# Performance work log

Measured on AMD Instinct MI355X. Metric: run time of the kernel, lower is better.

Reference implementation:

```python
import jax, jax.numpy as jnp
import numpy as np
import math

H_HEADS = 4
SQRT_2_PI = math.sqrt(2.0 / math.pi)


def _gelu_tanh(x):
    return 0.5 * x * (1.0 + jnp.tanh(SQRT_2_PI * (x + 0.044715 * x ** 3)))


def _ln(x, g, b, eps=1e-5):
    mu = jnp.mean(x, axis=-1, keepdims=True)
    var = jnp.var(x, axis=-1, keepdims=True)
    return g * (x - mu) * jax.lax.rsqrt(var + eps) + b


def _forward(support_emb_mat, query_t, support_t, cls_embed, t_freq, t_phase,
             Wq, bq, Wk, bk, Wv, bv, Wo, bo, ln1_g, ln1_b, time_w,
             W1, b1, W2, b2, ln2_g, ln2_b, Wc, bc, bn_g, bn_b):
    B, F, MD = support_emb_mat.shape
    Q = query_t.shape[1]
    S = F + 1
    H = H_HEADS
    D = MD * H
    dph = D // H
    L = Wq.shape[0]
    BQ = B * Q

    # [CLS] + support sequence, feature-tiled to model_dim*num_heads
    cls = jnp.broadcast_to(cls_embed, (B, 1, MD))
    seq = jnp.concatenate([cls, support_emb_mat], axis=1)          # [B,S,MD]
    x = jnp.tile(seq, (1, 1, H))                                    # [B,S,D]
    x = jnp.broadcast_to(x[:, None], (B, Q, S, D)).reshape(BQ, S, D)

    # time sequence: [query_t_q, support_t...] per (b,q)
    sup = jnp.broadcast_to(support_t[:, None, :], (B, Q, F))
    t_seq = jnp.concatenate([query_t[..., None], sup], axis=-1).reshape(BQ, S)
    t_diff = t_seq[:, :, None] - t_seq[:, None, :]                  # [BQ,S,S]
    # time encoder: cos(t*freq + phase) -> [BQ,S,S,TD]
    t_emb = jnp.cos(t_diff[..., None] * t_freq + t_phase)

    # scale as in source: (dim_per_head // num_heads) ** -0.5
    scale = (dph // H) ** (-0.5)

    for l in range(L):
        bias = t_emb @ time_w[l]                                    # [BQ,S,S]
        add = jnp.tile(bias, (H, 1, 1))                             # [BQ*H,S,S]
        res = x
        # raw row-major reshape to (BQ*H, S, dph) exactly as torch .view
        q = (x @ Wq[l] + bq[l]).reshape(BQ * H, S, dph)
        k = (x @ Wk[l] + bk[l]).reshape(BQ * H, S, dph)
        v = (x @ Wv[l] + bv[l]).reshape(BQ * H, S, dph)
        attn = jax.nn.softmax(jnp.einsum('bsd,btd->bst', q, k) * scale + add, axis=-1)
        ctx = jnp.einsum('bst,btd->bsd', attn, v).reshape(BQ, S, D)
        out = _ln(res + ctx @ Wo[l] + bo[l], ln1_g[l], ln1_b[l])
        ffn = _gelu_tanh(out @ W1[l] + b1[l]) @ W2[l] + b2[l]
        x = _ln(out + ffn, ln2_g[l], ln2_b[l])

    # compress: Linear -> BatchNorm1d over seq channels (train mode) -> LeakyReLU
    h = x @ Wc + bc                                                 # [BQ,S,MD]
    mu = jnp.mean(h, axis=(0, 2), keepdims=True)
    var = jnp.var(h, axis=(0, 2), keepdims=True)
    h = bn_g[None, :, None] * (h - mu) * jax.lax.rsqrt(var + 1e-5) + bn_b[None, :, None]
    h = jnp.where(h >= 0, h, 0.01 * h)                              # LeakyReLU
    return h[:, 0, :].reshape(B, Q, MD)


def setup_inputs() -> dict:
    key = jax.random.key(0)
    ks = jax.random.split(key, 24)
    B, Q, F, MD = 128, 32, 7, 128
    H, L, FFN, TD = 4, 6, 2048, 32
    S = F + 1
    D = MD * H

    def nrm(k, shape, s=0.02):
        return jax.random.normal(k, shape, jnp.float32) * s

    inp = {
        'support_emb_mat': jax.random.normal(ks[0], (B, F, MD), jnp.float32),
        'query_t': jax.random.uniform(ks[1], (B, Q), jnp.float32) * 100.0,
        'support_t': jax.random.uniform(ks[2], (B, F), jnp.float32) * 100.0,
        'cls_embed': jax.random.uniform(ks[3], (1, MD), jnp.float32),
        't_freq': nrm(ks[4], (TD,), 1.0),
        't_phase': nrm(ks[5], (TD,), 1.0),
        'Wq': nrm(ks[6], (L, D, D)), 'bq': jnp.zeros((L, D)),
        'Wk': nrm(ks[7], (L, D, D)), 'bk': jnp.zeros((L, D)),
        'Wv': nrm(ks[8], (L, D, D)), 'bv': jnp.zeros((L, D)),
        'Wo': nrm(ks[9], (L, D, D)), 'bo': jnp.zeros((L, D)),
        'ln1_g': jnp.ones((L, D)), 'ln1_b': jnp.zeros((L, D)),
        'time_w': jnp.ones((L, TD)) * 0.001,
        'W1': nrm(ks[10], (L, D, FFN)), 'b1': jnp.zeros((L, FFN)),
        'W2': nrm(ks[11], (L, FFN, D)), 'b2': jnp.zeros((L, D)),
        'ln2_g': jnp.ones((L, D)), 'ln2_b': jnp.zeros((L, D)),
        'Wc': nrm(ks[12], (D, MD)), 'bc': jnp.zeros((MD,)),
        'bn_g': jnp.ones((S,)), 'bn_b': jnp.zeros((S,)),
    }
    return inp


def reference(support_emb_mat, query_t, support_t, cls_embed, t_freq, t_phase,
              Wq, bq, Wk, bk, Wv, bv, Wo, bo, ln1_g, ln1_b, time_w,
              W1, b1, W2, b2, ln2_g, ln2_b, Wc, bc, bn_g, bn_b):
    return _forward(support_emb_mat, query_t, support_t, cls_embed, t_freq, t_phase,
                    Wq, bq, Wk, bk, Wv, bv, Wo, bo, ln1_g, ln1_b, time_w,
                    W1, b1, W2, b2, ln2_g, ln2_b, Wc, bc, bn_g, bn_b)
```

## Files before the change

### kernel.cpp

```cpp
#include <hip/hip_runtime.h>
#include <hip/hip_bf16.h>

typedef _Float16 f16;
typedef __attribute__((ext_vector_type(8))) _Float16 f16x8;
typedef __attribute__((ext_vector_type(4))) _Float16 f16x4;
typedef __attribute__((ext_vector_type(4))) float f32x4;

#define DEVI __device__ __forceinline__

DEVI float ldf(const void* p, size_t i, int isf32) {
    if (isf32) return ((const float*)p)[i];
    unsigned int u = ((const unsigned short*)p)[i];
    union { unsigned int b; float f; } c; c.b = u << 16;
    return c.f;
}

DEVI void gld_lds16(const f16* g, f16* l) {
    __builtin_amdgcn_global_load_lds(
        (__attribute__((address_space(1))) void*)(g),
        (__attribute__((address_space(3))) void*)(l), 16, 0, 0);
}

__global__ void detect_dtype(const void* qt, int* flag) {
    if (threadIdx.x == 0 && blockIdx.x == 0) {
        const unsigned int* w = (const unsigned int*)qt;
        int cnt = 0;
        for (int i = 0; i < 64; ++i) {
            unsigned int lo = w[i] & 0xFFFFu;
            union { unsigned int b; float f; } c; c.b = lo << 16;
            if (c.f >= 1e-4f && c.f <= 100.5f) ++cnt;
        }
        *flag = (cnt >= 32) ? 0 : 1;
    }
}

__global__ __launch_bounds__(256)
void cvt_in(const void* __restrict__ src, float* __restrict__ dst, int n,
            const int* __restrict__ flag) {
    const int f32 = *flag;
    int i = blockIdx.x * 256 + threadIdx.x;
    if (i < n) dst[i] = ldf(src, i, f32);
}

__global__ __launch_bounds__(256)
void fill_out(float* out, float v) {
    out[blockIdx.x * 256 + threadIdx.x] = v;
}

template<int EPI>
__global__ __launch_bounds__(256, 4)
void gemm_bt(const f16* __restrict__ Ag, const f16* __restrict__ BTg,
             const float* __restrict__ biasg, const f16* __restrict__ resg,
             void* __restrict__ outg,
             int NT, int NTZ, int MCHUNK, int MT, int N, int K, int lda,
             long zsB, long zsBias, long zsC)
{
    const int tid  = threadIdx.x;
    const int w    = tid >> 6, lane = tid & 63;
    const int wm   = w >> 1,   wn   = w & 1;

    const int id    = blockIdx.x;
    const int pc    = MCHUNK * NTZ;
    const int chunk = id / pc;
    const int rem   = id - chunk * pc;
    const int mloc  = rem % MCHUNK;
    const int ynz   = rem / MCHUNK;
    const int z     = ynz / NT;
    const int tmB   = (chunk * MCHUNK + mloc) * (128 * MT);
    const int tn    = (ynz - z * NT) * 128;

    const f16*   BT   = BTg + (size_t)z * zsB;
    const float* bias = biasg + (size_t)z * zsBias;
    const size_t zoffC = (size_t)z * zsC;

    __shared__ __align__(16) f16 smA[16][64][8];
    __shared__ __align__(16) f16 smB[16][64][8];

    const int r16 = lane & 15, q4 = lane >> 4;
    const int iters = K >> 6;

    for (int ms = 0; ms < MT; ++ms) {
        const int tm = tmB + ms * 128;

        f32x4 acc[4][4];
#pragma unroll
        for (int i = 0; i < 4; ++i)
#pragma unroll
            for (int j = 0; j < 4; ++j) acc[i][j] = (f32x4)0.0f;

        const f16* ga[4]; const f16* gb[4];
#pragma unroll
        for (int it = 0; it < 4; ++it) {
            int sb = w * 4 + it, mt = sb >> 1, ks = sb & 1;
            ga[it] = Ag + (size_t)(tm + mt * 16 + r16) * lda + ks * 32 + q4 * 8;
            gb[it] = BT + (size_t)(tn + mt * 16 + r16) * K   + ks * 32 + q4 * 8;
        }

        for (int kt = 0; kt < iters; ++kt) {
#pragma unroll
            for (int it = 0; it < 4; ++it) {
                int sb = w * 4 + it;
                gld_lds16(ga[it], &smA[sb][0][0]);
                gld_lds16(gb[it], &smB[sb][0][0]);
                ga[it] += 64; gb[it] += 64;
            }
            __syncthreads();
#pragma unroll
            for (int ks = 0; ks < 2; ++ks) {
                f16x8 af[4], bf[4];
#pragma unroll
                for (int i = 0; i < 4; ++i) {
                    af[i] = *(const f16x8*)&smA[(wm * 4 + i) * 2 + ks][lane][0];
                    bf[i] = *(const f16x8*)&smB[(wn * 4 + i) * 2 + ks][lane][0];
                }
#pragma unroll
                for (int i = 0; i < 4; ++i)
#pragma unroll
                    for (int j = 0; j < 4; ++j)
                        acc[i][j] = __builtin_amdgcn_mfma_f32_16x16x32_f16(
                            af[i], bf[j], acc[i][j], 0, 0, 0);
            }
            __syncthreads();
        }

        const int rowBase = tm + wm * 64;
        const int colBase = tn + wn * 64;
#pragma unroll
        for (int j = 0; j < 4; ++j) {
            const int col = colBase + j * 16 + r16;
            const float bv = bias[col];
#pragma unroll
            for (int i = 0; i < 4; ++i) {
                const int row0 = rowBase + i * 16 + q4 * 4;
#pragma unroll
                for (int r = 0; r < 4; ++r) {
                    const int row = row0 + r;
                    const size_t off = (size_t)row * N + col;
                    float v = acc[i][j][r] + bv;
                    if constexpr (EPI == 0) {
                        ((f16*)outg)[zoffC + off] = (f16)v;
                    } else if constexpr (EPI == 1) {
                        v += (float)resg[off];
                        ((f16*)outg)[off] = (f16)v;
                    } else if constexpr (EPI == 2) {
                        float t  = v + 0.044715f * v * v * v;
                        float u  = 1.5957691216057308f * t;
                        float e  = __expf(u);
                        float th = 1.0f - 2.0f / (e + 1.0f);
                        ((f16*)outg)[off] = (f16)(0.5f * v * (1.0f + th));
                    } else {
                        ((float*)outg)[off] = v;
                    }
                }
            }
        }
    }
}

__global__ __launch_bounds__(256)
void attn_kernel(const f16* __restrict__ qg, const f16* __restrict__ kg,
                 const f16* __restrict__ vg, const float* __restrict__ biasL,
                 f16* __restrict__ cg, int small)
{
    const int w = threadIdx.x >> 6, lane = threadIdx.x & 63;
    const int j = blockIdx.x * 4 + w;
    __shared__ __align__(16) f16 sQ[4][8][136];
    __shared__ __align__(16) f16 sK[4][8][136];
    __shared__ __align__(16) f16 sV[4][8][136];
    __shared__ float sP[4][8][8];

    const size_t base  = (size_t)j * 1024;
    const size_t ibase = small ? ((size_t)(j >> 7) * 4096 + (size_t)(j & 3) * 1024)
                               : base;
#pragma unroll
    for (int t = 0; t < 2; ++t) {
        int flat = (t * 64 + lane) * 8;
        int r = flat >> 7, c = flat & 127;
        *(f16x8*)&sQ[w][r][c] = *(const f16x8*)(qg + ibase + flat);
        *(f16x8*)&sK[w][r][c] = *(const f16x8*)(kg + ibase + flat);
        *(f16x8*)&sV[w][r][c] = *(const f16x8*)(vg + ibase + flat);
    }
    __syncthreads();

    const int i = lane >> 3, jj = lane & 7;
    float d = 0.f;
#pragma unroll
    for (int c = 0; c < 16; ++c) {
        f16x8 qv = *(const f16x8*)&sQ[w][i][c * 8];
        f16x8 kv = *(const f16x8*)&sK[w][jj][c * 8];
#pragma unroll
        for (int e = 0; e < 8; ++e) d += (float)qv[e] * (float)kv[e];
    }
    float s = d * 0.17677669529663687f + biasL[(size_t)(j & 4095) * 64 + lane];
    float mx = s;
    mx = fmaxf(mx, __shfl_xor(mx, 1, 64));
    mx = fmaxf(mx, __shfl_xor(mx, 2, 64));
    mx = fmaxf(mx, __shfl_xor(mx, 4, 64));
    float p = __expf(s - mx);
    float sum = p;
    sum += __shfl_xor(sum, 1, 64);
    sum += __shfl_xor(sum, 2, 64);
    sum += __shfl_xor(sum, 4, 64);
    sP[w][i][jj] = p / sum;
    __syncthreads();

#pragma unroll
    for (int t2 = 0; t2 < 8; ++t2) {
        float ap[8];
#pragma unroll
        for (int e = 0; e < 8; ++e) ap[e] = sP[w][t2][e];
#pragma unroll
        for (int h = 0; h < 2; ++h) {
            int flat = (t2 * 2 + h) * 64 + lane;
            int dd = flat & 127;
            float o = 0.f;
#pragma unroll
            for (int e = 0; e < 8; ++e) o += ap[e] * (float)sV[w][e][dd];
            cg[base + flat] = (f16)o;
        }
    }
}

__global__ __launch_bounds__(256)
void ln_kernel(const f16* __restrict__ X, const float* __restrict__ g,
               const float* __restrict__ b, f16* __restrict__ Y)
{
    const int w = threadIdx.x >> 6, lane = threadIdx.x & 63;
    const int row = blockIdx.x * 4 + w;
    f16x8 v = *(const f16x8*)(X + (size_t)row * 512 + lane * 8);
    float vf[8]; float s = 0.f, ss = 0.f;
#pragma unroll
    for (int e = 0; e < 8; ++e) { vf[e] = (float)v[e]; s += vf[e]; ss += vf[e] * vf[e]; }
#pragma unroll
    for (int m = 1; m <= 32; m <<= 1) {
        s  += __shfl_xor(s, m, 64);
        ss += __shfl_xor(ss, m, 64);
    }
    const float mu  = s * (1.0f / 512.0f);
    const float var = ss * (1.0f / 512.0f) - mu * mu;
    const float rs  = rsqrtf(var + 1e-5f);
    f32x4 g0 = *(const f32x4*)(g + lane * 8), g1 = *(const f32x4*)(g + lane * 8 + 4);
    f32x4 b0 = *(const f32x4*)(b + lane * 8), b1 = *(const f32x4*)(b + lane * 8 + 4);
    f16x8 y;
#pragma unroll
    for (int e = 0; e < 4; ++e) {
        y[e]     = (f16)(g0[e] * (vf[e]     - mu) * rs + b0[e]);
        y[e + 4] = (f16)(g1[e] * (vf[e + 4] - mu) * rs + b1[e]);
    }
    *(f16x8*)(Y + (size_t)row * 512 + lane * 8) = y;
}

__global__ __launch_bounds__(256)
void build_x0(const void* __restrict__ sup, const void* __restrict__ cls,
              f16* __restrict__ xb, const int* __restrict__ flag)
{
    const int f32 = *flag;
    const size_t idx = ((size_t)blockIdx.x * 256 + threadIdx.x) * 4;
    const int row = (int)(idx >> 9), col0 = (int)(idx & 511);
    const int s = row & 7, b = row >> 8;
    f16x4 o;
#pragma unroll
    for (int e = 0; e < 4; ++e) {
        const int md = (col0 + e) & 127;
        float v = (s == 0) ? ldf(cls, md, f32)
                           : ldf(sup, ((size_t)b * 7 + (s - 1)) * 128 + md, f32);
        o[e] = (f16)v;
    }
    *(f16x4*)(xb + idx) = o;
}

__global__ __launch_bounds__(256)
void build_x0s(const void* __restrict__ sup, const void* __restrict__ cls,
               f16* __restrict__ xs, const int* __restrict__ flag)
{
    const int f32 = *flag;
    const size_t idx = ((size_t)blockIdx.x * 256 + threadIdx.x) * 4;
    const int row = (int)(idx >> 9), col0 = (int)(idx & 511);
    const int s = row & 7, b = row >> 3;
    f16x4 o;
#pragma unroll
    for (int e = 0; e < 4; ++e) {
        const int md = (col0 + e) & 127;
        float v = (s == 0) ? ldf(cls, md, f32)
                           : ldf(sup, ((size_t)b * 7 + (s - 1)) * 128 + md, f32);
        o[e] = (f16)v;
    }
    *(f16x4*)(xs + idx) = o;
}

__global__ __launch_bounds__(256)
void bias_kernel(const void* __restrict__ qt, const void* __restrict__ st,
                 const void* __restrict__ freq, const void* __restrict__ phase,
                 const void* __restrict__ tw, float* __restrict__ biasAll,
                 const int* __restrict__ flag)
{
    const int f32 = *flag;
    const int lane = threadIdx.x & 63;
    const int bq = blockIdx.x * 4 + (threadIdx.x >> 6);
    const int b = bq >> 5, qq = bq & 31;
    const int i = lane >> 3, jj = lane & 7;
    const float ti = (i  == 0) ? ldf(qt, b * 32 + qq, f32) : ldf(st, b * 7 + i  - 1, f32);
    const float tj = (jj == 0) ? ldf(qt, b * 32 + qq, f32) : ldf(st, b * 7 + jj - 1, f32);
    const float td = ti - tj;
    float a[6] = {0.f, 0.f, 0.f, 0.f, 0.f, 0.f};
    for (int t = 0; t < 32; ++t) {
        float c = __cosf(td * ldf(freq, t, f32) + ldf(phase, t, f32));
#pragma unroll
        for (int l = 0; l < 6; ++l) a[l] += c * ldf(tw, l * 32 + t, f32);
    }
#pragma unroll
    for (int l = 0; l < 6; ++l)
        biasAll[(size_t)l * (4096 * 64) + (size_t)bq * 64 + lane] = a[l];
}

__global__ __launch_bounds__(256)
void transpose_cvt(const void* __restrict__ W, f16* __restrict__ WT,
                   int K, int N, long zsW, long zsWT, const int* __restrict__ flag)
{
    const int f32 = *flag;
    const size_t zoff = (size_t)blockIdx.z * zsW;
    f16* WTz = WT + (size_t)blockIdx.z * zsWT;
    __shared__ float tile[64][65];
    const int tn = blockIdx.x * 64, tk = blockIdx.y * 64;
#pragma unroll
    for (int t = 0; t < 16; ++t) {
        int idx = t * 256 + threadIdx.x;
        int r = idx >> 6, c = idx & 63;
        tile[r][c] = ldf(W, zoff + (size_t)(tk + r) * N + tn + c, f32);
    }
    __syncthreads();
#pragma unroll
    for (int t = 0; t < 16; ++t) {
        int idx = t * 256 + threadIdx.x;
        int r = idx >> 6, c = idx & 63;
        WTz[(size_t)(tn + r) * K + tk + c] = (f16)tile[c][r];
    }
}

__global__ __launch_bounds__(256)
void gather_qkvb(const void* __restrict__ bq, const void* __restrict__ bk,
                 const void* __restrict__ bv, float* __restrict__ dst,
                 const int* __restrict__ flag)
{
    const int f32 = *flag;
    int i = blockIdx.x * 256 + threadIdx.x;
    if (i < 9216) {
        int z = i / 3072, rem = i % 3072;
        const void* src = (z == 0) ? bq : ((z == 1) ? bk : bv);
        dst[i] = ldf(src, rem, f32);
    }
}

__global__ __launch_bounds__(256)
void bn_reduce(const float* __restrict__ h0, float* __restrict__ stats)
{
    const int t = blockIdx.x * 256 + threadIdx.x;
    float s = 0.f, ss = 0.f;
#pragma unroll
    for (int k = 0; k < 8; ++k) {
        float v = h0[t + k * 65536];
        s += v; ss += v * v;
    }
#pragma unroll
    for (int m = 1; m <= 32; m <<= 1) {
        s  += __shfl_xor(s, m, 64);
        ss += __shfl_xor(ss, m, 64);
    }
    __shared__ float ls[8];
    const int w = threadIdx.x >> 6, lane = threadIdx.x & 63;
    if (lane == 0) { ls[w] = s; ls[4 + w] = ss; }
    __syncthreads();
    if (threadIdx.x == 0) {
        atomicAdd(&stats[0], ls[0] + ls[1] + ls[2] + ls[3]);
        atomicAdd(&stats[1], ls[4] + ls[5] + ls[6] + ls[7]);
    }
}

__global__ __launch_bounds__(256)
void bn_apply(const float* __restrict__ h0, const float* __restrict__ stats,
              const float* __restrict__ bnp, float* __restrict__ out)
{
    const int t = blockIdx.x * 256 + threadIdx.x;
    const float mu  = stats[0] * (1.0f / 524288.0f);
    const float var = stats[1] * (1.0f / 524288.0f) - mu * mu;
    const float rs  = rsqrtf(var + 1e-5f);
    float v = bnp[0] * (h0[t] - mu) * rs + bnp[8];
    v = (v >= 0.f) ? v : 0.01f * v;
    out[t] = v;
}

extern "C" void kernel_launch(void* const* d_in, const int* in_sizes, int n_in,
                              void* d_out, int out_size, void* d_ws, size_t ws_size,
                              hipStream_t stream)
{
    (void)in_sizes; (void)n_in; (void)out_size;
    const void* sup   = d_in[0];
    const void* qt    = d_in[1];
    const void* st    = d_in[2];
    const void* cls   = d_in[3];
    const void* freq  = d_in[4];
    const void* phase = d_in[5];
    const void* Wq = d_in[6];  const void* bqv = d_in[7];
    const void* Wk = d_in[8];  const void* bkv = d_in[9];
    const void* Wv = d_in[10]; const void* bvv = d_in[11];
    const void* Wo = d_in[12]; const void* bo  = d_in[13];
    const void* ln1g = d_in[14]; const void* ln1b = d_in[15];
    const void* tw = d_in[16];
    const void* W1 = d_in[17]; const void* b1 = d_in[18];
    const void* W2 = d_in[19]; const void* b2 = d_in[20];
    const void* ln2g = d_in[21]; const void* ln2b = d_in[22];
    const void* Wc = d_in[23]; const void* bc = d_in[24];
    const void* bng = d_in[25]; const void* bnb = d_in[26];

    const size_t NEEDED = 245658240;
    if (ws_size < NEEDED) {
        fill_out<<<2048, 256, 0, stream>>>((float*)d_out, 999.0f);
        return;
    }

    char* ws = (char*)d_ws;
    f16*   wt      = (f16*)(ws + 0);
    float* biasAll = (float*)(ws + 37879808);
    float* qkvb    = (float*)(ws + 44171264);
    float* prm     = (float*)(ws + 44208128);
    float* stats   = (float*)(ws + 44331584);
    int*   flag    = (int*)  (ws + 44331592);
    f16*   xb      = (f16*)(ws + 44331648);
    f16*   ob      = (f16*)(ws + 77886080);
    char*  region  = ws + 111440512;
    f16*   qb      = (f16*)(region);
    f16*   kb      = (f16*)(region + 33554432);
    f16*   vb      = (f16*)(region + 67108864);
    f16*   cb      = (f16*)(region + 100663296);
    f16*   qs      = (f16*)(region);
    f16*   xs      = (f16*)(region + 100663296);
    f16*   pl1     = (f16*)(region);
    f16*   fbuf    = (f16*)(region);
    float* h0      = (float*)(region);

    detect_dtype<<<1, 64, 0, stream>>>(qt, flag);

    cvt_in<<<12, 256, 0, stream>>>(bo,   prm + 0,     3072,  flag);
    cvt_in<<<48, 256, 0, stream>>>(b1,   prm + 3072,  12288, flag);
    cvt_in<<<12, 256, 0, stream>>>(b2,   prm + 15360, 3072,  flag);
    cvt_in<<<1,  256, 0, stream>>>(bc,   prm + 18432, 128,   flag);
    cvt_in<<<12, 256, 0, stream>>>(ln1g, prm + 18560, 3072,  flag);
    cvt_in<<<12, 256, 0, stream>>>(ln1b, prm + 21632, 3072,  flag);
    cvt_in<<<12, 256, 0, stream>>>(ln2g, prm + 24704, 3072,  flag);
    cvt_in<<<12, 256, 0, stream>>>(ln2b, prm + 27776, 3072,  flag);
    cvt_in<<<1,  256, 0, stream>>>(bng,  prm + 30848, 8,     flag);
    cvt_in<<<1,  256, 0, stream>>>(bnb,  prm + 30856, 8,     flag);

    transpose_cvt<<<dim3(8, 8, 6),  256, 0, stream>>>(Wq, wt + 0,        512, 512,  262144, 262144, flag);
    transpose_cvt<<<dim3(8, 8, 6),  256, 0, stream>>>(Wk, wt + 1572864,  512, 512,  262144, 262144, flag);
    transpose_cvt<<<dim3(8, 8, 6),  256, 0, stream>>>(Wv, wt + 3145728,  512, 512,  262144, 262144, flag);
    transpose_cvt<<<dim3(8, 8, 6),  256, 0, stream>>>(Wo, wt + 4718592,  512, 512,  262144, 262144, flag);
    transpose_cvt<<<dim3(32, 8, 6), 256, 0, stream>>>(W1, wt + 6291456,  512, 2048, 1048576, 1048576, flag);
    transpose_cvt<<<dim3(8, 32, 6), 256, 0, stream>>>(W2, wt + 12582912, 2048, 512, 1048576, 1048576, flag);
    transpose_cvt<<<dim3(2, 8, 1),  256, 0, stream>>>(Wc, wt + 18874368, 512, 128,  0, 0, flag);
    gather_qkvb<<<36, 256, 0, stream>>>(bqv, bkv, bvv, qkvb, flag);
    build_x0<<<16384, 256, 0, stream>>>(sup, cls, xb, flag);
    build_x0s<<<512, 256, 0, stream>>>(sup, cls, xs, flag);
    bias_kernel<<<1024, 256, 0, stream>>>(qt, st, freq, phase, tw, biasAll, flag);
    hipMemsetAsync(stats, 0, 8, stream);

    for (int l = 0; l < 6; ++l) {
        if (l == 0) {
            gemm_bt<0><<<48, 256, 0, stream>>>(
                xs, wt, qkvb, nullptr, qs,
                4, 12, 4, 2, 512, 512, 512, 1572864, 3072, 524288);
            attn_kernel<<<4096, 256, 0, stream>>>(
                qs, qs + 524288, qs + 1048576, biasAll, cb, 1);
        } else {
            gemm_bt<0><<<1536, 256, 0, stream>>>(
                xb, wt + l * 262144, qkvb + l * 512, nullptr, qb,
                4, 12, 32, 2, 512, 512, 512, 1572864, 3072, 16777216);
            attn_kernel<<<4096, 256, 0, stream>>>(
                qb, kb, vb, biasAll + (size_t)l * 262144, cb, 0);
        }
        gemm_bt<1><<<512, 256, 0, stream>>>(
            cb, wt + 4718592 + l * 262144, prm + 0 + l * 512, xb, pl1,
            4, 4, 32, 2, 512, 512, 512, 0, 0, 0);
        ln_kernel<<<8192, 256, 0, stream>>>(pl1, prm + 18560 + l * 512, prm + 21632 + l * 512, ob);
        gemm_bt<2><<<2048, 256, 0, stream>>>(
            ob, wt + 6291456 + l * 1048576, prm + 3072 + l * 2048, nullptr, fbuf,
            16, 16, 32, 2, 2048, 512, 512, 0, 0, 0);
        gemm_bt<1><<<512, 256, 0, stream>>>(
            fbuf, wt + 12582912 + l * 1048576, prm + 15360 + l * 512, ob, xb,
            4, 4, 32, 2, 512, 2048, 2048, 0, 0, 0);
        ln_kernel<<<8192, 256, 0, stream>>>(xb, prm + 24704 + l * 512, prm + 27776 + l * 512, xb);
    }

    gemm_bt<3><<<32, 256, 0, stream>>>(
        xb, wt + 18874368, prm + 18432, nullptr, h0,
        1, 1, 32, 1, 128, 512, 4096 , 0, 0, 0);
    bn_reduce<<<256, 256, 0, stream>>>(h0, stats);
    bn_apply<<<2048, 256, 0, stream>>>(h0, stats, prm + 30848, (float*)d_out);
}
```

Measured before the change: 3.135 ms.

## Double-buffer GEMM LDS tiles with async prefetch and retune grid splits

Rewrites the gemm_bt main loop to use two LDS buffers with K-step 32. The global-to-LDS load for the next step, including the next M sub-tile, is issued before computing on the current buffer, with explicit waitcnt and barriers. The goal is to overlap memory latency with MFMA work instead of fully serialising load and compute. Several launches also change their MCHUNK/MT split to use twice as many blocks with one M sub-tile each. This gives more parallelism but less prefetch carry-over across M sub-tiles, and adds barrier overhead per smaller K step.

```diff
diff --git a/kernel.cpp b/kernel.cpp
--- a/kernel.cpp
+++ b/kernel.cpp
@@ -73,11 +73,28 @@
     const float* bias = biasg + (size_t)z * zsBias;
     const size_t zoffC = (size_t)z * zsC;
 
-    __shared__ __align__(16) f16 smA[16][64][8];
-    __shared__ __align__(16) f16 smB[16][64][8];
+    __shared__ __align__(16) f16 smA[2][8][64][8];
+    __shared__ __align__(16) f16 smB[2][8][64][8];
 
     const int r16 = lane & 15, q4 = lane >> 4;
-    const int iters = K >> 6;
+    const int iters = K >> 5;
+
+    const f16* gA0 = Ag + (size_t)(tmB + (2 * w)     * 16 + r16) * lda + q4 * 8;
+    const f16* gA1 = gA0 + (size_t)16 * lda;
+    const f16* gB0 = BT + (size_t)(tn  + (2 * w)     * 16 + r16) * K   + q4 * 8;
+    const f16* gB1 = gB0 + (size_t)16 * K;
+
+    auto issue = [&](int msN, int ktN, int buf) {
+        const size_t aoff = (size_t)msN * 128 * lda + (size_t)ktN * 32;
+        const size_t boff = (size_t)ktN * 32;
+        gld_lds16(gA0 + aoff, &smA[buf][2 * w][0][0]);
+        gld_lds16(gA1 + aoff, &smA[buf][2 * w + 1][0][0]);
+        gld_lds16(gB0 + boff, &smB[buf][2 * w][0][0]);
+        gld_lds16(gB1 + boff, &smB[buf][2 * w + 1][0][0]);
+    };
+
+    issue(0, 0, 0);
+    int stage = 0;
 
     for (int ms = 0; ms < MT; ++ms) {
         const int tm = tmB + ms * 128;
@@ -88,39 +105,32 @@
 #pragma unroll
             for (int j = 0; j < 4; ++j) acc[i][j] = (f32x4)0.0f;
 
-        const f16* ga[4]; const f16* gb[4];
-#pragma unroll
-        for (int it = 0; it < 4; ++it) {
-            int sb = w * 4 + it, mt = sb >> 1, ks = sb & 1;
-            ga[it] = Ag + (size_t)(tm + mt * 16 + r16) * lda + ks * 32 + q4 * 8;
-            gb[it] = BT + (size_t)(tn + mt * 16 + r16) * K   + ks * 32 + q4 * 8;
-        }
-
-        for (int kt = 0; kt < iters; ++kt) {
-#pragma unroll
-            for (int it = 0; it < 4; ++it) {
-                int sb = w * 4 + it;
-                gld_lds16(ga[it], &smA[sb][0][0]);
-                gld_lds16(gb[it], &smB[sb][0][0]);
-                ga[it] += 64; gb[it] += 64;
+        for (int kt = 0; kt < iters; ++kt, ++stage) {
+            const int cur = stage & 1;
+            __builtin_amdgcn_s_barrier();
+            int ktN = kt + 1, msN = ms;
+            if (ktN == iters) { ktN = 0; ++msN; }
+            if (msN < MT) {
+                issue(msN, ktN, cur ^ 1);
+                __builtin_amdgcn_s_waitcnt(0x0F74);
+            } else {
+                __builtin_amdgcn_s_waitcnt(0x0F70);
             }
-            __syncthreads();
-#pragma unroll
-            for (int ks = 0; ks < 2; ++ks) {
-                f16x8 af[4], bf[4];
-#pragma unroll
-                for (int i = 0; i < 4; ++i) {
-                    af[i] = *(const f16x8*)&smA[(wm * 4 + i) * 2 + ks][lane][0];
-                    bf[i] = *(const f16x8*)&smB[(wn * 4 + i) * 2 + ks][lane][0];
-                }
-#pragma unroll
-                for (int i = 0; i < 4; ++i)
-#pragma unroll
-                    for (int j = 0; j < 4; ++j)
-                        acc[i][j] = __builtin_amdgcn_mfma_f32_16x16x32_f16(
-                            af[i], bf[j], acc[i][j], 0, 0, 0);
+            __builtin_amdgcn_s_barrier();
+            __asm__ __volatile__("" ::: "memory");
+
+            f16x8 af[4], bf[4];
+#pragma unroll
+            for (int i = 0; i < 4; ++i) {
+                af[i] = *(const f16x8*)&smA[cur][wm * 4 + i][lane][0];
+                bf[i] = *(const f16x8*)&smB[cur][wn * 4 + i][lane][0];
             }
-            __syncthreads();
+#pragma unroll
+            for (int i = 0; i < 4; ++i)
+#pragma unroll
+                for (int j = 0; j < 4; ++j)
+                    acc[i][j] = __builtin_amdgcn_mfma_f32_16x16x32_f16(
+                        af[i], bf[j], acc[i][j], 0, 0, 0);
         }
 
         const int rowBase = tm + wm * 64;
@@ -466,9 +476,9 @@
 
     for (int l = 0; l < 6; ++l) {
         if (l == 0) {
-            gemm_bt<0><<<48, 256, 0, stream>>>(
+            gemm_bt<0><<<96, 256, 0, stream>>>(
                 xs, wt, qkvb, nullptr, qs,
-                4, 12, 4, 2, 512, 512, 512, 1572864, 3072, 524288);
+                4, 12, 8, 1, 512, 512, 512, 1572864, 3072, 524288);
             attn_kernel<<<4096, 256, 0, stream>>>(
                 qs, qs + 524288, qs + 1048576, biasAll, cb, 1);
         } else {
@@ -478,16 +488,16 @@
             attn_kernel<<<4096, 256, 0, stream>>>(
                 qb, kb, vb, biasAll + (size_t)l * 262144, cb, 0);
         }
-        gemm_bt<1><<<512, 256, 0, stream>>>(
+        gemm_bt<1><<<1024, 256, 0, stream>>>(
             cb, wt + 4718592 + l * 262144, prm + 0 + l * 512, xb, pl1,
-            4, 4, 32, 2, 512, 512, 512, 0, 0, 0);
+            4, 4, 64, 1, 512, 512, 512, 0, 0, 0);
         ln_kernel<<<8192, 256, 0, stream>>>(pl1, prm + 18560 + l * 512, prm + 21632 + l * 512, ob);
         gemm_bt<2><<<2048, 256, 0, stream>>>(
             ob, wt + 6291456 + l * 1048576, prm + 3072 + l * 2048, nullptr, fbuf,
             16, 16, 32, 2, 2048, 512, 512, 0, 0, 0);
-        gemm_bt<1><<<512, 256, 0, stream>>>(
+        gemm_bt<1><<<1024, 256, 0, stream>>>(
             fbuf, wt + 12582912 + l * 1048576, prm + 15360 + l * 512, ob, xb,
-            4, 4, 32, 2, 512, 2048, 2048, 0, 0, 0);
+            4, 4, 64, 1, 512, 2048, 2048, 0, 0, 0);
         ln_kernel<<<8192, 256, 0, stream>>>(xb, prm + 24704 + l * 512, prm + 27776 + l * 512, xb);
     }
 
```

New measurement: 3.248 ms. 3.6% more time.
